# Performance work log

Hardware: AMD Instinct MI355X
Metric: run time of the kernel (lower is better)

## Reference

```python
import jax, jax.numpy as jnp
import numpy as np

N_NODES = 1_000_000
N_EDGES = 8_000_000


def _gcn_conv(x, src, dst, norm, W, b, n):
    # PyG GCNConv: x' = D^-1/2 (A + I) D^-1/2 (x W) + b
    h = x @ W                          # [N, out]
    msg = h[src] * norm[:, None]       # gather + edge-wise scale, [E', out]
    agg = jax.ops.segment_sum(msg, dst, num_segments=n)
    return agg + b


def setup_inputs() -> dict:
    key = jax.random.key(0)
    ks = jax.random.split(key, 6)
    F, H, O = 3, 32, 2
    x = jax.random.normal(ks[0], (N_NODES, F), dtype=jnp.float32)
    edge_index = jax.random.randint(ks[1], (2, N_EDGES), 0, N_NODES, dtype=jnp.int32)
    W1 = jax.random.normal(ks[2], (F, H), dtype=jnp.float32) * 0.3
    b1 = jnp.zeros((H,), jnp.float32)
    W2 = jax.random.normal(ks[3], (H, H), dtype=jnp.float32) * 0.15
    b2 = jnp.zeros((H,), jnp.float32)
    W3 = jax.random.normal(ks[4], (H, O), dtype=jnp.float32) * 0.15
    b3 = jnp.zeros((O,), jnp.float32)
    return {"x": x, "edge_index": edge_index, "W1": W1, "b1": b1,
            "W2": W2, "b2": b2, "W3": W3, "b3": b3}


def reference(x, edge_index, W1, b1, W2, b2, W3, b3):
    n = x.shape[0]
    loop = jnp.arange(n, dtype=edge_index.dtype)
    src = jnp.concatenate([edge_index[0], loop])  # add self-loops
    dst = jnp.concatenate([edge_index[1], loop])
    # symmetric degree normalization on A + I
    deg = jax.ops.segment_sum(jnp.ones_like(dst, dtype=x.dtype), dst, num_segments=n)
    dinv = jnp.where(deg > 0, jax.lax.rsqrt(deg), 0.0)
    norm = dinv[src] * dinv[dst]                  # [E + N]

    h = jax.nn.relu(_gcn_conv(x, src, dst, norm, W1, b1, n))
    h = jax.nn.relu(_gcn_conv(h, src, dst, norm, W2, b2, n))
    return h @ W3 + b3
```

## Files before the change

kernel.cpp:

```cpp
#include <hip/hip_runtime.h>


typedef unsigned int u32;
typedef unsigned char u8;

static __device__ __forceinline__ u32 bf16rn(float f) {
    u32 u = __float_as_uint(f);
    u += 0x7FFFu + ((u >> 16) & 1u);
    return u >> 16;
}
static __device__ __forceinline__ u32 pack_bf16(float a, float b) {
    return bf16rn(a) | (bf16rn(b) << 16);
}
static __device__ __forceinline__ float bflo(u32 w) { return __uint_as_float(w << 16); }
static __device__ __forceinline__ float bfhi(u32 w) { return __uint_as_float(w & 0xFFFF0000u); }
static __device__ __forceinline__ float rlane(float v, int l) {
    return __uint_as_float(__builtin_amdgcn_readlane(__float_as_uint(v), l));
}

__global__ void zero_u32_kernel(u32* __restrict__ p, int n) {
    int i = blockIdx.x * blockDim.x + threadIdx.x;
    if (i < n) p[i] = 0u;
}

__global__ void deg_pos_kernel(const int* __restrict__ dst, u32* __restrict__ cnt,
                               u8* __restrict__ pos8, int E) {
    int e = blockIdx.x * blockDim.x + threadIdx.x;
    if (e >= E) return;
    u32 old = atomicAdd(&cnt[dst[e]], 1u);
    pos8[e] = (u8)old;
}

__global__ void scan_k1(const u32* __restrict__ cnt, u32* __restrict__ rowptr,
                        u32* __restrict__ bsum, int N) {
    __shared__ u32 sdata[256];
    int tid = threadIdx.x;
    int base = blockIdx.x * 4096 + tid * 16;
    u32 v[16], pre[16], s = 0;
#pragma unroll
    for (int k = 0; k < 16; ++k) {
        int idx = base + k;
        v[k] = (idx < N) ? cnt[idx] : 0u;
        pre[k] = s; s += v[k];
    }
    sdata[tid] = s; __syncthreads();
    for (int off = 1; off < 256; off <<= 1) {
        u32 t = (tid >= off) ? sdata[tid - off] : 0u;
        __syncthreads();
        sdata[tid] += t;
        __syncthreads();
    }
    u32 excl = sdata[tid] - s;
#pragma unroll
    for (int k = 0; k < 16; ++k) {
        int idx = base + k;
        if (idx < N) rowptr[idx] = excl + pre[k];
    }
    if (tid == 255) bsum[blockIdx.x] = sdata[255];
}

__global__ void scan_k2(const u32* __restrict__ bsum, u32* __restrict__ boff, int NB) {
    __shared__ u32 sdata[256];
    int tid = threadIdx.x;
    u32 s = (tid < NB) ? bsum[tid] : 0u;
    sdata[tid] = s; __syncthreads();
    for (int off = 1; off < 256; off <<= 1) {
        u32 t = (tid >= off) ? sdata[tid - off] : 0u;
        __syncthreads();
        sdata[tid] += t;
        __syncthreads();
    }
    if (tid < NB) boff[tid] = sdata[tid] - s;
}

__global__ void finalize_kernel(u32* __restrict__ rowptr, const u32* __restrict__ boff,
                                const u32* __restrict__ cnt, const float* __restrict__ x,
                                float* __restrict__ dinv, float4* __restrict__ u4, int N) {
    int i = blockIdx.x * blockDim.x + threadIdx.x;
    if (i >= N) return;
    u32 r = rowptr[i] + boff[i >> 12];
    rowptr[i] = r;
    if (i == N - 1) rowptr[N] = r + cnt[i];
    float iv = rsqrtf((float)cnt[i] + 1.0f);
    dinv[i] = iv;
    u4[i] = make_float4(x[i * 3 + 0] * iv, x[i * 3 + 1] * iv, x[i * 3 + 2] * iv, 0.0f);
}

__global__ void scatter_kernel(const int* __restrict__ src, const int* __restrict__ dst,
                               const u8* __restrict__ pos8, const u32* __restrict__ rowptr,
                               int* __restrict__ srec, int E) {
    int e = blockIdx.x * blockDim.x + threadIdx.x;
    if (e >= E) return;
    u32 slot = rowptr[dst[e]] + (u32)pos8[e];
    srec[slot] = src[e];
}

__global__ void l1_kernel(const u32* __restrict__ rowptr, const int* __restrict__ srec,
                          const float4* __restrict__ u4, const float* __restrict__ dinv,
                          const float* __restrict__ W1, const float* __restrict__ b1,
                          u32* __restrict__ g1u, int N) {
    __shared__ float sW1[96];
    __shared__ float sb1[32];
    if (threadIdx.x < 96) sW1[threadIdx.x] = W1[threadIdx.x];
    if (threadIdx.x < 32) sb1[threadIdx.x] = b1[threadIdx.x];
    __syncthreads();
    int i = blockIdx.x * blockDim.x + threadIdx.x;
    if (i >= N) return;
    float iv = dinv[i];
    float4 u = u4[i];
    float a0 = u.x, a1 = u.y, a2 = u.z;
    u32 beg = rowptr[i], end = rowptr[i + 1];
    for (u32 t = beg; t < end; ++t) {
        float4 us = u4[srec[t]];
        a0 += us.x; a1 += us.y; a2 += us.z;
    }
    a0 *= iv; a1 *= iv; a2 *= iv;
    u32 packed[16];
#pragma unroll
    for (int jj = 0; jj < 16; ++jj) {
        int j0 = 2 * jj, j1 = 2 * jj + 1;
        float v0 = fmaf(a0, sW1[j0], fmaf(a1, sW1[32 + j0], fmaf(a2, sW1[64 + j0], sb1[j0])));
        float v1 = fmaf(a0, sW1[j1], fmaf(a1, sW1[32 + j1], fmaf(a2, sW1[64 + j1], sb1[j1])));
        v0 = fmaxf(v0, 0.0f) * iv;
        v1 = fmaxf(v1, 0.0f) * iv;
        packed[jj] = pack_bf16(v0, v1);
    }
    uint4* dp = (uint4*)(g1u + (size_t)i * 16);
    const uint4* pp = (const uint4*)packed;
    dp[0] = pp[0]; dp[1] = pp[1]; dp[2] = pp[2]; dp[3] = pp[3];
}

__global__ void l2_fused_kernel(const u32* __restrict__ rowptr, const int* __restrict__ srec,
                                const u32* __restrict__ g1u, const float* __restrict__ dinv,
                                const float* __restrict__ W2, const float* __restrict__ b2,
                                const float* __restrict__ W3, const float* __restrict__ b3,
                                float* __restrict__ out, int N) {
    const int lane = threadIdx.x & 63;
    const int j    = lane & 31;
    const int half = lane >> 5;
    const int fl   = lane & 7;
    const int esub = lane >> 3;

    float w2col[32];
#pragma unroll
    for (int k = 0; k < 32; ++k) w2col[k] = W2[k * 32 + j];
    const float b2j = b2[j];
    const float w3j = W3[2 * j + half];
    const float b3h = b3[half];

    const int nWaves = (gridDim.x * blockDim.x) >> 6;
    const int waveId = (blockIdx.x * blockDim.x + threadIdx.x) >> 6;

    for (int node = waveId; node < N; node += nWaves) {
        u32 beg = rowptr[node], end = rowptr[node + 1];
        float a0, a1, a2, a3;
        {
            uint2 w = *(const uint2*)(g1u + (size_t)node * 16 + 2 * fl);
            bool sf = (esub == 0);
            a0 = sf ? bflo(w.x) : 0.0f;
            a1 = sf ? bfhi(w.x) : 0.0f;
            a2 = sf ? bflo(w.y) : 0.0f;
            a3 = sf ? bfhi(w.y) : 0.0f;
        }
        for (u32 chunk = beg; chunk < end; chunk += 64) {
            int navail = (int)(end - chunk); if (navail > 64) navail = 64;
            int sv = (lane < navail) ? srec[chunk + lane] : 0;
            for (int q = 0; q < navail; q += 8) {
                int eidx = q + esub;
                int s = __shfl(sv, eidx);
                if (eidx < navail) {
                    uint2 w = *(const uint2*)(g1u + (size_t)s * 16 + 2 * fl);
                    a0 += bflo(w.x); a1 += bfhi(w.x);
                    a2 += bflo(w.y); a3 += bfhi(w.y);
                }
            }
        }
        a0 += __shfl_xor(a0, 8);  a1 += __shfl_xor(a1, 8);
        a2 += __shfl_xor(a2, 8);  a3 += __shfl_xor(a3, 8);
        a0 += __shfl_xor(a0, 16); a1 += __shfl_xor(a1, 16);
        a2 += __shfl_xor(a2, 16); a3 += __shfl_xor(a3, 16);
        a0 += __shfl_xor(a0, 32); a1 += __shfl_xor(a1, 32);
        a2 += __shfl_xor(a2, 32); a3 += __shfl_xor(a3, 32);
        float iv = dinv[node];
        a0 *= iv; a1 *= iv; a2 *= iv; a3 *= iv;

        float h = b2j;
#pragma unroll
        for (int k4 = 0; k4 < 8; ++k4) {
            h = fmaf(rlane(a0, k4), w2col[4 * k4 + 0], h);
            h = fmaf(rlane(a1, k4), w2col[4 * k4 + 1], h);
            h = fmaf(rlane(a2, k4), w2col[4 * k4 + 2], h);
            h = fmaf(rlane(a3, k4), w2col[4 * k4 + 3], h);
        }
        h = fmaxf(h, 0.0f);
        float p = h * w3j;
        p += __shfl_xor(p, 1);  p += __shfl_xor(p, 2);
        p += __shfl_xor(p, 4);  p += __shfl_xor(p, 8);
        p += __shfl_xor(p, 16);
        if (j == 0) out[(size_t)node * 2 + half] = p + b3h;
    }
}

extern "C" void kernel_launch(void* const* d_in, const int* in_sizes, int n_in,
                              void* d_out, int out_size, void* d_ws, size_t ws_size,
                              hipStream_t stream) {
    const float* x  = (const float*)d_in[0];
    const int*   ei = (const int*)d_in[1];
    const float* W1 = (const float*)d_in[2];
    const float* b1 = (const float*)d_in[3];
    const float* W2 = (const float*)d_in[4];
    const float* b2 = (const float*)d_in[5];
    const float* W3 = (const float*)d_in[6];
    const float* b3 = (const float*)d_in[7];
    float* out = (float*)d_out;

    const int N = in_sizes[0] / 3;
    const int E = in_sizes[1] / 2;
    const int* src = ei;
    const int* dst = ei + E;

    auto align256 = [](size_t v) { return (v + 255) & ~(size_t)255; };
    char* ws = (char*)d_ws;
    size_t off = 0;
    int*    srec   = (int*)   (ws + off); off = align256(off + (size_t)E * 4);
    u32*    g1u    = (u32*)   (ws + off); off = align256(off + (size_t)N * 16 * 4);
    float4* u4     = (float4*)(ws + off); off = align256(off + (size_t)N * 16);
    u8*     pos8   = (u8*)    (ws + off); off = align256(off + (size_t)E);
    u32*    rowptr = (u32*)   (ws + off); off = align256(off + (size_t)(N + 1) * 4);
    u32*    cnt    = (u32*)   (ws + off); off = align256(off + (size_t)N * 4);
    float*  dinv   = (float*) (ws + off); off = align256(off + (size_t)N * 4);
    u32*    bsum   = (u32*)   (ws + off); off = align256(off + 256 * 4);
    u32*    boff   = (u32*)   (ws + off); off = align256(off + 256 * 4);
    (void)ws_size;

    const int B = 256;
    const int NB = (N + 4095) / 4096;

    zero_u32_kernel<<<(N + B - 1) / B, B, 0, stream>>>(cnt, N);
    deg_pos_kernel<<<(E + B - 1) / B, B, 0, stream>>>(dst, cnt, pos8, E);
    scan_k1<<<NB, B, 0, stream>>>(cnt, rowptr, bsum, N);
    scan_k2<<<1, B, 0, stream>>>(bsum, boff, NB);
    finalize_kernel<<<(N + B - 1) / B, B, 0, stream>>>(rowptr, boff, cnt, x, dinv, u4, N);
    scatter_kernel<<<(E + B - 1) / B, B, 0, stream>>>(src, dst, pos8, rowptr, srec, E);
    l1_kernel<<<(N + B - 1) / B, B, 0, stream>>>(rowptr, srec, u4, dinv, W1, b1, g1u, N);
    l2_fused_kernel<<<2048, B, 0, stream>>>(rowptr, srec, g1u, dinv, W2, b2, W3, b3, out, N);
}
```

Baseline: 1.294 ms.

## Process two nodes per wavefront in layer-2 fused aggregation kernel

Layer-2 aggregation now maps two destination nodes to each 64-lane wavefront, one per 32-lane half, instead of one node per wave. Each half gathers 4 edges per step and reduces inside its own half, so the cross-half shuffle goes away. The final output is written as a float2 per node. This targets the idle lanes and reduction overhead caused by average degree around 9, at the cost of divergence when the two paired nodes have different degrees and more shuffle-based broadcasts in place of readlane.

```diff
diff --git a/kernel.cpp b/kernel.cpp
--- a/kernel.cpp
+++ b/kernel.cpp
@@ -14,9 +14,6 @@
 }
 static __device__ __forceinline__ float bflo(u32 w) { return __uint_as_float(w << 16); }
 static __device__ __forceinline__ float bfhi(u32 w) { return __uint_as_float(w & 0xFFFF0000u); }
-static __device__ __forceinline__ float rlane(float v, int l) {
-    return __uint_as_float(__builtin_amdgcn_readlane(__float_as_uint(v), l));
-}
 
 __global__ void zero_u32_kernel(u32* __restrict__ p, int n) {
     int i = blockIdx.x * blockDim.x + threadIdx.x;
@@ -136,38 +133,44 @@
                                 const float* __restrict__ W3, const float* __restrict__ b3,
                                 float* __restrict__ out, int N) {
     const int lane = threadIdx.x & 63;
-    const int j    = lane & 31;
-    const int half = lane >> 5;
-    const int fl   = lane & 7;
-    const int esub = lane >> 3;
+    const int l32  = lane & 31;
+    const int h    = lane >> 5;
+    const int fl   = l32 & 7;
+    const int esub = l32 >> 3;
 
     float w2col[32];
 #pragma unroll
-    for (int k = 0; k < 32; ++k) w2col[k] = W2[k * 32 + j];
-    const float b2j = b2[j];
-    const float w3j = W3[2 * j + half];
-    const float b3h = b3[half];
+    for (int k = 0; k < 32; ++k) w2col[k] = W2[k * 32 + l32];
+    const float b2j = b2[l32];
+    const float w30 = W3[2 * l32 + 0];
+    const float w31 = W3[2 * l32 + 1];
+    const float b30 = b3[0], b31 = b3[1];
 
     const int nWaves = (gridDim.x * blockDim.x) >> 6;
     const int waveId = (blockIdx.x * blockDim.x + threadIdx.x) >> 6;
 
-    for (int node = waveId; node < N; node += nWaves) {
-        u32 beg = rowptr[node], end = rowptr[node + 1];
-        float a0, a1, a2, a3;
-        {
+    for (int base = waveId * 2; base < N; base += nWaves * 2) {
+        const int node = base + h;
+        const bool valid = node < N;
+        u32 beg = 0; int deg = 0;
+        if (valid) {
+            uint2 rp = *(const uint2*)(rowptr + node);
+            beg = rp.x; deg = (int)(rp.y - rp.x);
+        }
+        float a0 = 0.0f, a1 = 0.0f, a2 = 0.0f, a3 = 0.0f;
+        if (valid && esub == 0) {
             uint2 w = *(const uint2*)(g1u + (size_t)node * 16 + 2 * fl);
-            bool sf = (esub == 0);
-            a0 = sf ? bflo(w.x) : 0.0f;
-            a1 = sf ? bfhi(w.x) : 0.0f;
-            a2 = sf ? bflo(w.y) : 0.0f;
-            a3 = sf ? bfhi(w.y) : 0.0f;
-        }
-        for (u32 chunk = beg; chunk < end; chunk += 64) {
-            int navail = (int)(end - chunk); if (navail > 64) navail = 64;
-            int sv = (lane < navail) ? srec[chunk + lane] : 0;
-            for (int q = 0; q < navail; q += 8) {
+            a0 = bflo(w.x); a1 = bfhi(w.x); a2 = bflo(w.y); a3 = bfhi(w.y);
+        }
+        int mdeg = max(deg, __shfl_xor(deg, 32));
+        for (int q0 = 0; q0 < mdeg; q0 += 32) {
+            int navail = deg - q0;
+            navail = navail < 0 ? 0 : (navail > 32 ? 32 : navail);
+            int sv = (l32 < navail) ? srec[beg + q0 + l32] : 0;
+            int mnav = max(navail, __shfl_xor(navail, 32));
+            for (int q = 0; q < mnav; q += 4) {
                 int eidx = q + esub;
-                int s = __shfl(sv, eidx);
+                int s = __shfl(sv, eidx, 32);
                 if (eidx < navail) {
                     uint2 w = *(const uint2*)(g1u + (size_t)s * 16 + 2 * fl);
                     a0 += bflo(w.x); a1 += bfhi(w.x);
@@ -179,25 +182,26 @@
         a2 += __shfl_xor(a2, 8);  a3 += __shfl_xor(a3, 8);
         a0 += __shfl_xor(a0, 16); a1 += __shfl_xor(a1, 16);
         a2 += __shfl_xor(a2, 16); a3 += __shfl_xor(a3, 16);
-        a0 += __shfl_xor(a0, 32); a1 += __shfl_xor(a1, 32);
-        a2 += __shfl_xor(a2, 32); a3 += __shfl_xor(a3, 32);
-        float iv = dinv[node];
+        float iv = valid ? dinv[node] : 0.0f;
         a0 *= iv; a1 *= iv; a2 *= iv; a3 *= iv;
 
-        float h = b2j;
-#pragma unroll
-        for (int k4 = 0; k4 < 8; ++k4) {
-            h = fmaf(rlane(a0, k4), w2col[4 * k4 + 0], h);
-            h = fmaf(rlane(a1, k4), w2col[4 * k4 + 1], h);
-            h = fmaf(rlane(a2, k4), w2col[4 * k4 + 2], h);
-            h = fmaf(rlane(a3, k4), w2col[4 * k4 + 3], h);
-        }
-        h = fmaxf(h, 0.0f);
-        float p = h * w3j;
-        p += __shfl_xor(p, 1);  p += __shfl_xor(p, 2);
-        p += __shfl_xor(p, 4);  p += __shfl_xor(p, 8);
-        p += __shfl_xor(p, 16);
-        if (j == 0) out[(size_t)node * 2 + half] = p + b3h;
+        float hh = b2j;
+#pragma unroll
+        for (int f = 0; f < 8; ++f) {
+            hh = fmaf(__shfl(a0, f, 32), w2col[4 * f + 0], hh);
+            hh = fmaf(__shfl(a1, f, 32), w2col[4 * f + 1], hh);
+            hh = fmaf(__shfl(a2, f, 32), w2col[4 * f + 2], hh);
+            hh = fmaf(__shfl(a3, f, 32), w2col[4 * f + 3], hh);
+        }
+        hh = fmaxf(hh, 0.0f);
+        float p0 = hh * w30, p1 = hh * w31;
+        p0 += __shfl_xor(p0, 1);  p1 += __shfl_xor(p1, 1);
+        p0 += __shfl_xor(p0, 2);  p1 += __shfl_xor(p1, 2);
+        p0 += __shfl_xor(p0, 4);  p1 += __shfl_xor(p1, 4);
+        p0 += __shfl_xor(p0, 8);  p1 += __shfl_xor(p1, 8);
+        p0 += __shfl_xor(p0, 16); p1 += __shfl_xor(p1, 16);
+        if (valid && l32 == 0)
+            *(float2*)(out + (size_t)node * 2) = make_float2(p0 + b30, p1 + b31);
     }
 }
 
```

Result: faster. 1.205 ms (-6.8%).
